# Kernel tuning notes

Measured on AMD Instinct MI355X. Metric: run time of the kernel, lower is better.

The kernel has to match this reference:

```python
import jax, jax.numpy as jnp
import numpy as np

B, S, D, H = 4, 2048, 1024, 16
HD = D // H


def sinusoidal_pe(max_len, d_model):
    pos = np.arange(max_len)[:, None].astype(np.float32)
    div = np.exp(np.arange(0, d_model, 2).astype(np.float32) * (-np.log(10000.0) / d_model))
    pe = np.zeros((max_len, d_model), dtype=np.float32)
    pe[:, 0::2] = np.sin(pos * div)
    pe[:, 1::2] = np.cos(pos * div)
    return jnp.asarray(pe)


def setup_inputs() -> dict:
    key = jax.random.key(0)
    ks = jax.random.split(key, 9)
    s = 1.0 / np.sqrt(D)
    inp = {
        "x": jax.random.normal(ks[0], (B, S, D), dtype=jnp.float32),
        "Wq": jax.random.normal(ks[1], (D, D), dtype=jnp.float32) * s,
        "bq": jnp.zeros((D,), dtype=jnp.float32),
        "Wk": jax.random.normal(ks[2], (D, D), dtype=jnp.float32) * s,
        "bk": jnp.zeros((D,), dtype=jnp.float32),
        "Wv": jax.random.normal(ks[3], (D, D), dtype=jnp.float32) * s,
        "bv": jnp.zeros((D,), dtype=jnp.float32),
        "Wp": jax.random.normal(ks[4], (D, D), dtype=jnp.float32) * s,
        "bp": jnp.zeros((D,), dtype=jnp.float32),
        "pe": sinusoidal_pe(S, D),
    }
    return inp


def reference(x, Wq, bq, Wk, bk, Wv, bv, Wp, bp, pe):
    # positional encoding (eval mode: dropout is identity)
    xp = x + pe[None, :, :]  # [B,S,D]
    split = lambda t: t.reshape(B, S, H, HD).transpose(0, 2, 1, 3)  # [B,H,S,HD]
    q = split(xp @ Wq.T + bq)
    k = split(xp @ Wk.T + bk)
    v = split(xp @ Wv.T + bv)
    scores = jnp.einsum("bhqd,bhkd->bhqk", q, k) / jnp.sqrt(jnp.float32(HD))
    attn = jax.nn.softmax(scores, axis=-1)
    ctx = jnp.einsum("bhqk,bhkd->bhqd", attn, v)
    ctx = ctx.transpose(0, 2, 1, 3).reshape(B, S, D)
    return ctx @ Wp.T + bp
```

## Files before the change

kernel.cpp:

```cpp
#include <hip/hip_runtime.h>
#include <hip/hip_bf16.h>
#include <stdint.h>

#define B_  4
#define S_  2048
#define D_  1024
#define H_  16
#define HD_ 64

typedef __bf16 bfx8   __attribute__((ext_vector_type(8)));
typedef float  f32x4  __attribute__((ext_vector_type(4)));
typedef float  f32x16 __attribute__((ext_vector_type(16)));
typedef short  s16x4  __attribute__((ext_vector_type(4)));
typedef float  fl4    __attribute__((ext_vector_type(4)));
typedef unsigned int u32x2 __attribute__((ext_vector_type(2)));
typedef unsigned int u32x4 __attribute__((ext_vector_type(4)));

#define EXP2(x) __builtin_amdgcn_exp2f(x)

static __device__ __forceinline__ unsigned short f2bf(float f) {
    union { float f; unsigned int u; } v; v.f = f;
    unsigned int r = v.u + 0x7fffu + ((v.u >> 16) & 1u);
    return (unsigned short)(r >> 16);
}
static __device__ __forceinline__ unsigned int fbits(float f) {
    union { float f; unsigned int u; } v; v.f = f; return v.u;
}

#define GLD_LDS16(gp, lp) __builtin_amdgcn_global_load_lds( \
    (const __attribute__((address_space(1))) unsigned int*)(gp), \
    (__attribute__((address_space(3))) unsigned int*)(lp), 16, 0, 0)

__global__ __launch_bounds__(256) void prep_kernel(
    const float* __restrict__ x, const float* __restrict__ pe,
    const float* __restrict__ w0, const float* __restrict__ w1,
    const float* __restrict__ w2, const float* __restrict__ w3,
    unsigned short* __restrict__ xpb, unsigned short* __restrict__ wcat)
{
    const int blk = blockIdx.x;
    if (blk < 8192) {
        int i = (blk * 256 + threadIdx.x) * 4;
        fl4 xv = *(const fl4*)(x + i);
        fl4 pv = *(const fl4*)(pe + (i & (S_ * D_ - 1)));
        s16x4 r;
#pragma unroll
        for (int j = 0; j < 4; j++) r[j] = (short)f2bf(xv[j] + pv[j]);
        *(s16x4*)(xpb + i) = r;
    } else {
        const int bb = blk - 8192;
        const int wsel = bb >> 10;
        const float* src = wsel == 0 ? w0 : wsel == 1 ? w1 : wsel == 2 ? w2 : w3;
        int i = (((bb & 1023) * 256) + threadIdx.x) * 4;
        fl4 v = *(const fl4*)(src + i);
        s16x4 r;
#pragma unroll
        for (int j = 0; j < 4; j++) r[j] = (short)f2bf(v[j]);
        *(s16x4*)(wcat + (size_t)wsel * D_ * D_ + i) = r;
    }
}

__global__ __launch_bounds__(256, 2) void gemm_qkv(
    const unsigned short* __restrict__ A,
    const unsigned short* __restrict__ Bw,
    const float* __restrict__ bq, const float* __restrict__ bk,
    const float* __restrict__ bv,
    unsigned short* __restrict__ Qo, unsigned short* __restrict__ Ko,
    unsigned short* __restrict__ Vo, float qscale)
{
    constexpr int K = D_;
    __shared__ unsigned short As[128 * 32];
    __shared__ unsigned short Bs[128 * 32];
    const int hw  = blockIdx.x;
    const int xcd = hw & 7;
    const int i_  = hw >> 3;
    const int m0  = (i_ / 3) * 128;
    const int n0  = (xcd * 3 + i_ % 3) * 128;

    const int t  = threadIdx.x;
    const int l  = t & 63;
    const int w  = t >> 6;
    const int wr = (w >> 1) * 64;
    const int wc = (w & 1) * 64;
    const int lr = l & 15;
    const int lg = l >> 4;
    const int lk = lg * 8;

    const int e0 = t * 8;
    const int sr = e0 >> 5;
    const int sc = e0 & 31;
    const unsigned short* pA = A  + (size_t)(m0 + sr) * K + sc;
    const unsigned short* pB = Bw + (size_t)(n0 + sr) * K + sc;

    f32x4 acc[4][4] = {};

    for (int k0 = 0; k0 < K; k0 += 32) {
        __syncthreads();
        GLD_LDS16(pA + k0,                    As + e0);
        GLD_LDS16(pA + k0 + (size_t)64 * K,   As + 2048 + e0);
        GLD_LDS16(pB + k0,                    Bs + e0);
        GLD_LDS16(pB + k0 + (size_t)64 * K,   Bs + 2048 + e0);
        __syncthreads();
        bfx8 af[4], bf[4];
#pragma unroll
        for (int i = 0; i < 4; i++)
            af[i] = *(const bfx8*)(As + (wr + i * 16 + lr) * 32 + lk);
#pragma unroll
        for (int i = 0; i < 4; i++)
            bf[i] = *(const bfx8*)(Bs + (wc + i * 16 + lr) * 32 + lk);
#pragma unroll
        for (int i = 0; i < 4; i++)
#pragma unroll
            for (int j = 0; j < 4; j++)
                acc[i][j] = __builtin_amdgcn_mfma_f32_16x16x32_bf16(
                    af[i], bf[j], acc[i][j], 0, 0, 0);
    }

    const int sel = n0 >> 10;
    const float* bias = sel == 0 ? bq : sel == 1 ? bk : bv;
    const float osc = sel == 0 ? qscale : 1.0f;

#pragma unroll
    for (int i = 0; i < 4; i++) {
        const int row0 = m0 + wr + i * 16 + lg * 4;
#pragma unroll
        for (int j = 0; j < 4; j++) {
            const int colf = n0 + wc + j * 16 + lr;
            const int ocol = colf & 1023;
            const float bvv = bias[ocol];
            if (sel < 2) {
                unsigned short* C = sel == 0 ? Qo : Ko;
#pragma unroll
                for (int v = 0; v < 4; v++)
                    C[(size_t)(row0 + v) * D_ + ocol] = f2bf((acc[i][j][v] + bvv) * osc);
            } else {
                const int bidx = row0 >> 11;
                const int s0   = row0 & (S_ - 1);
                s16x4 r;
#pragma unroll
                for (int v = 0; v < 4; v++) r[v] = (short)f2bf(acc[i][j][v] + bvv);
                *(s16x4*)(Vo + (size_t)(bidx * D_ + ocol) * S_ + s0) = r;
            }
        }
    }
}

__global__ __launch_bounds__(256, 2) void gemm_out(
    const unsigned short* __restrict__ A,
    const unsigned short* __restrict__ Bw,
    const float* __restrict__ bias,
    float* __restrict__ Cout)
{
    constexpr int K = D_;
    constexpr int N = D_;
    __shared__ unsigned short As[128 * 32];
    __shared__ unsigned short Bs[128 * 32];
    const int hw = blockIdx.x;
    const int logical = (hw & 7) * 64 + (hw >> 3);
    const int m0 = (logical >> 3) * 128;
    const int n0 = (logical & 7) * 128;

    const int t  = threadIdx.x;
    const int l  = t & 63;
    const int w  = t >> 6;
    const int wr = (w >> 1) * 64;
    const int wc = (w & 1) * 64;
    const int lr = l & 15;
    const int lg = l >> 4;
    const int lk = lg * 8;

    const int e0 = t * 8;
    const int sr = e0 >> 5;
    const int sc = e0 & 31;
    const unsigned short* pA = A  + (size_t)(m0 + sr) * K + sc;
    const unsigned short* pB = Bw + (size_t)(n0 + sr) * K + sc;

    f32x4 acc[4][4] = {};

    for (int k0 = 0; k0 < K; k0 += 32) {
        __syncthreads();
        GLD_LDS16(pA + k0,                    As + e0);
        GLD_LDS16(pA + k0 + (size_t)64 * K,   As + 2048 + e0);
        GLD_LDS16(pB + k0,                    Bs + e0);
        GLD_LDS16(pB + k0 + (size_t)64 * K,   Bs + 2048 + e0);
        __syncthreads();
        bfx8 af[4], bf[4];
#pragma unroll
        for (int i = 0; i < 4; i++)
            af[i] = *(const bfx8*)(As + (wr + i * 16 + lr) * 32 + lk);
#pragma unroll
        for (int i = 0; i < 4; i++)
            bf[i] = *(const bfx8*)(Bs + (wc + i * 16 + lr) * 32 + lk);
#pragma unroll
        for (int i = 0; i < 4; i++)
#pragma unroll
            for (int j = 0; j < 4; j++)
                acc[i][j] = __builtin_amdgcn_mfma_f32_16x16x32_bf16(
                    af[i], bf[j], acc[i][j], 0, 0, 0);
    }

#pragma unroll
    for (int i = 0; i < 4; i++) {
        const int row0 = m0 + wr + i * 16 + lg * 4;
#pragma unroll
        for (int j = 0; j < 4; j++) {
            const int col = n0 + wc + j * 16 + lr;
            const float bv = bias[col];
#pragma unroll
            for (int v = 0; v < 4; v++)
                Cout[(size_t)(row0 + v) * N + col] = acc[i][j][v] + bv;
        }
    }
}

__global__ __launch_bounds__(256, 4) void attn_kernel(
    const unsigned short* __restrict__ Qb,
    const unsigned short* __restrict__ Kb,
    const unsigned short* __restrict__ Vt,
    unsigned short* __restrict__ Ctx)
{
    __shared__ __align__(16) unsigned short Ks[2][64 * 64];
    __shared__ __align__(16) unsigned short Vs[2][64 * 64];

    const int hw = blockIdx.x;
    const int logical = (hw & 7) * 128 + (hw >> 3);
    const int bh = logical >> 4;
    const int t  = threadIdx.x;
    const int l  = t & 63;
    const int w  = t >> 6;
    const int b  = bh >> 4;
    const int h  = bh & 15;
    const int lr = l & 31;
    const int hi = l >> 5;
    const int q0 = (logical & 15) * 128 + w * 32;

    const unsigned short* Qbase = Qb + (size_t)b * S_ * D_ + h * HD_;
    const unsigned short* Kbase = Kb + (size_t)b * S_ * D_ + h * HD_;
    const unsigned short* Vbase = Vt + (size_t)bh * HD_ * S_;

    const int r0  = t >> 3;
    const int cgs = (t & 7) ^ (r0 & 7);
    const unsigned short* Ksrc0 = Kbase + (size_t)r0 * D_ + cgs * 8;
    const unsigned short* Ksrc1 = Kbase + (size_t)(r0 + 32) * D_ + cgs * 8;
    const unsigned short* Vsrc0 = Vbase + (size_t)r0 * S_ + cgs * 8;
    const unsigned short* Vsrc1 = Vbase + (size_t)(r0 + 32) * S_ + cgs * 8;
    const int ld0 = t * 8, ld1 = t * 8 + 2048;

    GLD_LDS16(Ksrc0, &Ks[0][ld0]);
    GLD_LDS16(Ksrc1, &Ks[0][ld1]);
    GLD_LDS16(Vsrc0, &Vs[0][ld0]);
    GLD_LDS16(Vsrc1, &Vs[0][ld1]);

    bfx8 qf[4];
#pragma unroll
    for (int t4 = 0; t4 < 4; t4++)
        qf[t4] = *(const bfx8*)(Qbase + (size_t)(q0 + lr) * D_ + t4 * 16 + hi * 8);

    f32x16 acc0 = {}, acc1 = {};
    float l_r = 0.f;
    const int sw = lr & 7;

    int cur = 0;
    for (int ki = 0; ki < S_ / 64; ki++) {
        __syncthreads();
        if (ki + 1 < S_ / 64) {
            GLD_LDS16(Ksrc0 + (size_t)(ki + 1) * 64 * D_, &Ks[cur ^ 1][ld0]);
            GLD_LDS16(Ksrc1 + (size_t)(ki + 1) * 64 * D_, &Ks[cur ^ 1][ld1]);
            GLD_LDS16(Vsrc0 + (ki + 1) * 64,              &Vs[cur ^ 1][ld0]);
            GLD_LDS16(Vsrc1 + (ki + 1) * 64,              &Vs[cur ^ 1][ld1]);
        }
        const unsigned short* Kc = Ks[cur];
        const unsigned short* Vc = Vs[cur];

        f32x16 s0 = {}, s1 = {};
        __builtin_amdgcn_s_setprio(1);
#pragma unroll
        for (int t4 = 0; t4 < 4; t4++) {
            const int ch = ((t4 * 2 + hi) ^ sw) * 8;
            bfx8 a0 = *(const bfx8*)(Kc + lr * 64 + ch);
            bfx8 a1 = *(const bfx8*)(Kc + (32 + lr) * 64 + ch);
            s0 = __builtin_amdgcn_mfma_f32_32x32x16_bf16(a0, qf[t4], s0, 0, 0, 0);
            s1 = __builtin_amdgcn_mfma_f32_32x32x16_bf16(a1, qf[t4], s1, 0, 0, 0);
        }
        __builtin_amdgcn_s_setprio(0);

        float c0 = 0.f, c1 = 0.f, c2 = 0.f, c3 = 0.f;
#pragma unroll
        for (int r = 0; r < 16; r += 4) {
            float p0 = EXP2(s0[r]);     s0[r] = p0;     c0 += p0;
            float p1 = EXP2(s0[r + 1]); s0[r + 1] = p1; c1 += p1;
            float p2 = EXP2(s0[r + 2]); s0[r + 2] = p2; c2 += p2;
            float p3 = EXP2(s0[r + 3]); s0[r + 3] = p3; c3 += p3;
        }
#pragma unroll
        for (int r = 0; r < 16; r += 4) {
            float p0 = EXP2(s1[r]);     s1[r] = p0;     c0 += p0;
            float p1 = EXP2(s1[r + 1]); s1[r + 1] = p1; c1 += p1;
            float p2 = EXP2(s1[r + 2]); s1[r + 2] = p2; c2 += p2;
            float p3 = EXP2(s1[r + 3]); s1[r + 3] = p3; c3 += p3;
        }
        l_r += (c0 + c1) + (c2 + c3);

        unsigned pk0[8], pk1[8];
#pragma unroll
        for (int i = 0; i < 8; i++) {
            pk0[i] = __builtin_amdgcn_perm(fbits(s0[2 * i + 1]), fbits(s0[2 * i]), 0x07060302u);
            pk1[i] = __builtin_amdgcn_perm(fbits(s1[2 * i + 1]), fbits(s1[2 * i]), 0x07060302u);
        }

#pragma unroll
        for (int ks = 0; ks < 4; ks++) {
            const int c = (ks & 1) * 4;
            const unsigned pa0 = (ks >> 1) ? pk1[c]     : pk0[c];
            const unsigned pa1 = (ks >> 1) ? pk1[c + 1] : pk0[c + 1];
            const unsigned pa2 = (ks >> 1) ? pk1[c + 2] : pk0[c + 2];
            const unsigned pa3 = (ks >> 1) ? pk1[c + 3] : pk0[c + 3];
            u32x2 r02 = __builtin_amdgcn_permlane32_swap(pa0, pa2, false, false);
            u32x2 r13 = __builtin_amdgcn_permlane32_swap(pa1, pa3, false, false);
            u32x4 bfr;
            bfr[0] = r02[0];
            bfr[1] = r13[0];
            bfr[2] = r02[1];
            bfr[3] = r13[1];
            union { u32x4 u; bfx8 b; } cvt; cvt.u = bfr;

            const int ch = ((ks * 2 + hi) ^ sw) * 8;
            bfx8 v0 = *(const bfx8*)(Vc + lr * 64 + ch);
            bfx8 v1 = *(const bfx8*)(Vc + (32 + lr) * 64 + ch);
            __builtin_amdgcn_s_setprio(1);
            acc0 = __builtin_amdgcn_mfma_f32_32x32x16_bf16(v0, cvt.b, acc0, 0, 0, 0);
            acc1 = __builtin_amdgcn_mfma_f32_32x32x16_bf16(v1, cvt.b, acc1, 0, 0, 0);
            __builtin_amdgcn_s_setprio(0);
        }
        cur ^= 1;
    }

    const float l_tot = l_r + __shfl_xor(l_r, 32);
    const float rinv = 1.0f / l_tot;
    unsigned short* Cb = Ctx + (size_t)b * S_ * D_ + (size_t)(q0 + lr) * D_ + h * HD_;
#pragma unroll
    for (int dt = 0; dt < 2; dt++)
#pragma unroll
        for (int a = 0; a < 4; a++) {
            s16x4 rv;
#pragma unroll
            for (int v = 0; v < 4; v++)
                rv[v] = (short)f2bf((dt ? acc1[4 * a + v] : acc0[4 * a + v]) * rinv);
            *(s16x4*)(Cb + dt * 32 + 8 * a + 4 * hi) = rv;
        }
}

extern "C" void kernel_launch(void* const* d_in, const int* in_sizes, int n_in,
                              void* d_out, int out_size, void* d_ws, size_t ws_size,
                              hipStream_t stream)
{
    const float* x  = (const float*)d_in[0];
    const float* Wq = (const float*)d_in[1];
    const float* bq = (const float*)d_in[2];
    const float* Wk = (const float*)d_in[3];
    const float* bk = (const float*)d_in[4];
    const float* Wv = (const float*)d_in[5];
    const float* bv = (const float*)d_in[6];
    const float* Wp = (const float*)d_in[7];
    const float* bp = (const float*)d_in[8];
    const float* pe = (const float*)d_in[9];

    char* ws = (char*)d_ws;
    const size_t MD = (size_t)B_ * S_ * D_;
    unsigned short* xpb = (unsigned short*)ws; ws += MD * 2;
    unsigned short* wqb = (unsigned short*)ws; ws += (size_t)D_ * D_ * 2;
    unsigned short* wkb = (unsigned short*)ws; ws += (size_t)D_ * D_ * 2;
    unsigned short* wvb = (unsigned short*)ws; ws += (size_t)D_ * D_ * 2;
    unsigned short* wpb = (unsigned short*)ws; ws += (size_t)D_ * D_ * 2;
    unsigned short* qb  = (unsigned short*)ws; ws += MD * 2;
    unsigned short* kb  = (unsigned short*)ws; ws += MD * 2;
    unsigned short* vtb = (unsigned short*)ws; ws += MD * 2;
    unsigned short* ctb = (unsigned short*)ws; ws += MD * 2;

    prep_kernel<<<12288, 256, 0, stream>>>(x, pe, Wq, Wk, Wv, Wp, xpb, wqb);

    const float qscale = 0.125f * 1.44269504088896340736f;

    gemm_qkv<<<1536, 256, 0, stream>>>(xpb, wqb, bq, bk, bv, qb, kb, vtb, qscale);

    attn_kernel<<<1024, 256, 0, stream>>>(qb, kb, vtb, ctb);

    gemm_out<<<512, 256, 0, stream>>>(ctb, wpb, bp, (float*)d_out);
}
```

Before: 201.8 us.

## Replace both GEMMs with 256x256 double-buffered, swizzled, phased MFMA kernel

Replaces the 128x128 single-buffered QKV and output GEMMs with one templated kernel. It uses 256x256 tiles, 512 threads and a K step of 64. The LDS buffers are double-buffered with an XOR swizzle. Each k-step is split into four phases that interleave async global-to-LDS loads with MFMA bursts, using explicit barriers and s_setprio. The aim is more data reuse per LDS byte, fewer barriers and better overlap of loads with compute. The cost is fewer blocks: 128 for the output GEMM on a 256-CU part, and about 1.5 waves for QKV. The 128 KB of LDS also limits each CU to one block.

Measured after the change: 210.0 us. 4.1% more time.

```diff
diff --git a/kernel.cpp b/kernel.cpp
--- a/kernel.cpp
+++ b/kernel.cpp
@@ -30,6 +30,10 @@
 #define GLD_LDS16(gp, lp) __builtin_amdgcn_global_load_lds( \
     (const __attribute__((address_space(1))) unsigned int*)(gp), \
     (__attribute__((address_space(3))) unsigned int*)(lp), 16, 0, 0)
+
+#define MFMA16(a, b, c) __builtin_amdgcn_mfma_f32_16x16x32_bf16((a), (b), (c), 0, 0, 0)
+#define SBAR()  do { __builtin_amdgcn_sched_barrier(0); __builtin_amdgcn_s_barrier(); \
+                     __builtin_amdgcn_sched_barrier(0); } while (0)
 
 __global__ __launch_bounds__(256) void prep_kernel(
     const float* __restrict__ x, const float* __restrict__ pe,
@@ -59,157 +63,184 @@
     }
 }
 
-__global__ __launch_bounds__(256, 2) void gemm_qkv(
+template<int MODE>
+__global__ __launch_bounds__(512, 2) void gemm_8ph(
     const unsigned short* __restrict__ A,
     const unsigned short* __restrict__ Bw,
-    const float* __restrict__ bq, const float* __restrict__ bk,
-    const float* __restrict__ bv,
-    unsigned short* __restrict__ Qo, unsigned short* __restrict__ Ko,
-    unsigned short* __restrict__ Vo, float qscale)
+    const float* __restrict__ b0, const float* __restrict__ b1,
+    const float* __restrict__ b2,
+    unsigned short* __restrict__ O0, unsigned short* __restrict__ O1,
+    unsigned short* __restrict__ O2, float* __restrict__ Fo, float qscale)
 {
-    constexpr int K = D_;
-    __shared__ unsigned short As[128 * 32];
-    __shared__ unsigned short Bs[128 * 32];
+    constexpr int KK  = 1024;
+    constexpr int NKT = 16;
+    __shared__ __align__(16) unsigned short As[2][256 * 64];
+    __shared__ __align__(16) unsigned short Bs[2][256 * 64];
+
     const int hw  = blockIdx.x;
     const int xcd = hw & 7;
     const int i_  = hw >> 3;
-    const int m0  = (i_ / 3) * 128;
-    const int n0  = (xcd * 3 + i_ % 3) * 128;
-
-    const int t  = threadIdx.x;
-    const int l  = t & 63;
-    const int w  = t >> 6;
-    const int wr = (w >> 1) * 64;
-    const int wc = (w & 1) * 64;
-    const int lr = l & 15;
-    const int lg = l >> 4;
-    const int lk = lg * 8;
-
-    const int e0 = t * 8;
-    const int sr = e0 >> 5;
-    const int sc = e0 & 31;
-    const unsigned short* pA = A  + (size_t)(m0 + sr) * K + sc;
-    const unsigned short* pB = Bw + (size_t)(n0 + sr) * K + sc;
-
-    f32x4 acc[4][4] = {};
-
-    for (int k0 = 0; k0 < K; k0 += 32) {
-        __syncthreads();
-        GLD_LDS16(pA + k0,                    As + e0);
-        GLD_LDS16(pA + k0 + (size_t)64 * K,   As + 2048 + e0);
-        GLD_LDS16(pB + k0,                    Bs + e0);
-        GLD_LDS16(pB + k0 + (size_t)64 * K,   Bs + 2048 + e0);
-        __syncthreads();
-        bfx8 af[4], bf[4];
+    const int mt  = xcd * 4 + (i_ & 3);
+    const int nt  = i_ >> 2;
+    const int m0  = mt * 256;
+    const int n0  = nt * 256;
+
+    const int t   = threadIdx.x;
+    const int wid = t >> 6;
+    const int wm  = wid >> 2;
+    const int wn  = wid & 3;
+    const int l   = t & 63;
+    const int lr  = l & 15;
+    const int lg  = l >> 4;
+
+    const int srow  = t >> 3;
+    const int sslot = t & 7;
+
+#define STAGE_HALF(dst, X, R0, kn, half) do {                                   \
+    const int r0_ = (half) * 128 + srow;                                        \
+    const int r1_ = r0_ + 64;                                                   \
+    GLD_LDS16(X + (size_t)((R0) + r0_) * KK + (kn) + ((sslot ^ (r0_ & 7)) * 8), \
+              (dst) + 8 * t + (half) * 8192);                                   \
+    GLD_LDS16(X + (size_t)((R0) + r1_) * KK + (kn) + ((sslot ^ (r1_ & 7)) * 8), \
+              (dst) + 8 * t + (half) * 8192 + 4096);                            \
+} while (0)
+
+#define RD(buf, row, ks) \
+    (*(const bfx8*)((buf) + (row) * 64 + ((((ks) * 4 + lg) ^ ((row) & 7)) * 8)))
+
+    f32x4 acc[8][4] = {};
+    bfx8 af[4][2], bfa[2][2], bfb[2][2];
+
+    STAGE_HALF(As[0], A,  m0, 0, 0);
+    STAGE_HALF(As[0], A,  m0, 0, 1);
+    STAGE_HALF(Bs[0], Bw, n0, 0, 0);
+    STAGE_HALF(Bs[0], Bw, n0, 0, 1);
+
+    for (int kt = 0; kt < NKT; ++kt) {
+        const int c = kt & 1;
+        const unsigned short* Ac = As[c];
+        const unsigned short* Bc = Bs[c];
+        unsigned short* An = As[c ^ 1];
+        unsigned short* Bn = Bs[c ^ 1];
+        const int kn = ((kt + 1) & (NKT - 1)) * 64;
+
+        STAGE_HALF(An, A, m0, kn, 0);
+        asm volatile("s_waitcnt vmcnt(2)" ::: "memory");
+        SBAR();
+#pragma unroll
+        for (int i = 0; i < 4; i++) {
+            af[i][0] = RD(Ac, wm * 128 + i * 16 + lr, 0);
+            af[i][1] = RD(Ac, wm * 128 + i * 16 + lr, 1);
+        }
+#pragma unroll
+        for (int j = 0; j < 2; j++) {
+            bfa[j][0] = RD(Bc, wn * 64 + j * 16 + lr, 0);
+            bfa[j][1] = RD(Bc, wn * 64 + j * 16 + lr, 1);
+        }
+        __builtin_amdgcn_s_setprio(1);
 #pragma unroll
         for (int i = 0; i < 4; i++)
-            af[i] = *(const bfx8*)(As + (wr + i * 16 + lr) * 32 + lk);
+#pragma unroll
+            for (int j = 0; j < 2; j++) {
+                acc[i][j] = MFMA16(af[i][0], bfa[j][0], acc[i][j]);
+                acc[i][j] = MFMA16(af[i][1], bfa[j][1], acc[i][j]);
+            }
+        __builtin_amdgcn_s_setprio(0);
+        SBAR();
+
+#pragma unroll
+        for (int j = 0; j < 2; j++) {
+            bfb[j][0] = RD(Bc, wn * 64 + 32 + j * 16 + lr, 0);
+            bfb[j][1] = RD(Bc, wn * 64 + 32 + j * 16 + lr, 1);
+        }
+        STAGE_HALF(An, A, m0, kn, 1);
+        SBAR();
+        __builtin_amdgcn_s_setprio(1);
 #pragma unroll
         for (int i = 0; i < 4; i++)
-            bf[i] = *(const bfx8*)(Bs + (wc + i * 16 + lr) * 32 + lk);
+#pragma unroll
+            for (int j = 0; j < 2; j++) {
+                acc[i][2 + j] = MFMA16(af[i][0], bfb[j][0], acc[i][2 + j]);
+                acc[i][2 + j] = MFMA16(af[i][1], bfb[j][1], acc[i][2 + j]);
+            }
+        __builtin_amdgcn_s_setprio(0);
+        SBAR();
+
+#pragma unroll
+        for (int i = 0; i < 4; i++) {
+            af[i][0] = RD(Ac, wm * 128 + (4 + i) * 16 + lr, 0);
+            af[i][1] = RD(Ac, wm * 128 + (4 + i) * 16 + lr, 1);
+        }
+        STAGE_HALF(Bn, Bw, n0, kn, 0);
+        SBAR();
+        __builtin_amdgcn_s_setprio(1);
 #pragma unroll
         for (int i = 0; i < 4; i++)
 #pragma unroll
-            for (int j = 0; j < 4; j++)
-                acc[i][j] = __builtin_amdgcn_mfma_f32_16x16x32_bf16(
-                    af[i], bf[j], acc[i][j], 0, 0, 0);
+            for (int j = 0; j < 2; j++) {
+                acc[4 + i][j] = MFMA16(af[i][0], bfa[j][0], acc[4 + i][j]);
+                acc[4 + i][j] = MFMA16(af[i][1], bfa[j][1], acc[4 + i][j]);
+            }
+        __builtin_amdgcn_s_setprio(0);
+        SBAR();
+
+        STAGE_HALF(Bn, Bw, n0, kn, 1);
+        SBAR();
+        __builtin_amdgcn_s_setprio(1);
+#pragma unroll
+        for (int i = 0; i < 4; i++)
+#pragma unroll
+            for (int j = 0; j < 2; j++) {
+                acc[4 + i][2 + j] = MFMA16(af[i][0], bfb[j][0], acc[4 + i][2 + j]);
+                acc[4 + i][2 + j] = MFMA16(af[i][1], bfb[j][1], acc[4 + i][2 + j]);
+            }
+        __builtin_amdgcn_s_setprio(0);
+        SBAR();
     }
 
-    const int sel = n0 >> 10;
-    const float* bias = sel == 0 ? bq : sel == 1 ? bk : bv;
-    const float osc = sel == 0 ? qscale : 1.0f;
-
-#pragma unroll
-    for (int i = 0; i < 4; i++) {
-        const int row0 = m0 + wr + i * 16 + lg * 4;
-#pragma unroll
-        for (int j = 0; j < 4; j++) {
-            const int colf = n0 + wc + j * 16 + lr;
-            const int ocol = colf & 1023;
-            const float bvv = bias[ocol];
-            if (sel < 2) {
-                unsigned short* C = sel == 0 ? Qo : Ko;
+    if (MODE == 0) {
+        const int sel = n0 >> 10;
+        const float* bias = sel == 0 ? b0 : sel == 1 ? b1 : b2;
+        const float osc = sel == 0 ? qscale : 1.0f;
+#pragma unroll
+        for (int mi = 0; mi < 8; mi++) {
+            const int row0 = m0 + wm * 128 + mi * 16 + lg * 4;
+#pragma unroll
+            for (int ni = 0; ni < 4; ni++) {
+                const int colf = n0 + wn * 64 + ni * 16 + lr;
+                const int ocol = colf & 1023;
+                const float bvv = bias[ocol];
+                if (sel < 2) {
+                    unsigned short* C = sel == 0 ? O0 : O1;
+#pragma unroll
+                    for (int v = 0; v < 4; v++)
+                        C[(size_t)(row0 + v) * D_ + ocol] = f2bf((acc[mi][ni][v] + bvv) * osc);
+                } else {
+                    const int bidx = row0 >> 11;
+                    const int s0   = row0 & (S_ - 1);
+                    s16x4 r;
+#pragma unroll
+                    for (int v = 0; v < 4; v++) r[v] = (short)f2bf(acc[mi][ni][v] + bvv);
+                    *(s16x4*)(O2 + (size_t)(bidx * D_ + ocol) * S_ + s0) = r;
+                }
+            }
+        }
+    } else {
+#pragma unroll
+        for (int mi = 0; mi < 8; mi++) {
+            const int row0 = m0 + wm * 128 + mi * 16 + lg * 4;
+#pragma unroll
+            for (int ni = 0; ni < 4; ni++) {
+                const int col = n0 + wn * 64 + ni * 16 + lr;
+                const float bvv = b0[col];
 #pragma unroll
                 for (int v = 0; v < 4; v++)
-                    C[(size_t)(row0 + v) * D_ + ocol] = f2bf((acc[i][j][v] + bvv) * osc);
-            } else {
-                const int bidx = row0 >> 11;
-                const int s0   = row0 & (S_ - 1);
-                s16x4 r;
-#pragma unroll
-                for (int v = 0; v < 4; v++) r[v] = (short)f2bf(acc[i][j][v] + bvv);
-                *(s16x4*)(Vo + (size_t)(bidx * D_ + ocol) * S_ + s0) = r;
+                    Fo[(size_t)(row0 + v) * D_ + col] = acc[mi][ni][v] + bvv;
             }
         }
     }
-}
-
-__global__ __launch_bounds__(256, 2) void gemm_out(
-    const unsigned short* __restrict__ A,
-    const unsigned short* __restrict__ Bw,
-    const float* __restrict__ bias,
-    float* __restrict__ Cout)
-{
-    constexpr int K = D_;
-    constexpr int N = D_;
-    __shared__ unsigned short As[128 * 32];
-    __shared__ unsigned short Bs[128 * 32];
-    const int hw = blockIdx.x;
-    const int logical = (hw & 7) * 64 + (hw >> 3);
-    const int m0 = (logical >> 3) * 128;
-    const int n0 = (logical & 7) * 128;
-
-    const int t  = threadIdx.x;
-    const int l  = t & 63;
-    const int w  = t >> 6;
-    const int wr = (w >> 1) * 64;
-    const int wc = (w & 1) * 64;
-    const int lr = l & 15;
-    const int lg = l >> 4;
-    const int lk = lg * 8;
-
-    const int e0 = t * 8;
-    const int sr = e0 >> 5;
-    const int sc = e0 & 31;
-    const unsigned short* pA = A  + (size_t)(m0 + sr) * K + sc;
-    const unsigned short* pB = Bw + (size_t)(n0 + sr) * K + sc;
-
-    f32x4 acc[4][4] = {};
-
-    for (int k0 = 0; k0 < K; k0 += 32) {
-        __syncthreads();
-        GLD_LDS16(pA + k0,                    As + e0);
-        GLD_LDS16(pA + k0 + (size_t)64 * K,   As + 2048 + e0);
-        GLD_LDS16(pB + k0,                    Bs + e0);
-        GLD_LDS16(pB + k0 + (size_t)64 * K,   Bs + 2048 + e0);
-        __syncthreads();
-        bfx8 af[4], bf[4];
-#pragma unroll
-        for (int i = 0; i < 4; i++)
-            af[i] = *(const bfx8*)(As + (wr + i * 16 + lr) * 32 + lk);
-#pragma unroll
-        for (int i = 0; i < 4; i++)
-            bf[i] = *(const bfx8*)(Bs + (wc + i * 16 + lr) * 32 + lk);
-#pragma unroll
-        for (int i = 0; i < 4; i++)
-#pragma unroll
-            for (int j = 0; j < 4; j++)
-                acc[i][j] = __builtin_amdgcn_mfma_f32_16x16x32_bf16(
-                    af[i], bf[j], acc[i][j], 0, 0, 0);
-    }
-
-#pragma unroll
-    for (int i = 0; i < 4; i++) {
-        const int row0 = m0 + wr + i * 16 + lg * 4;
-#pragma unroll
-        for (int j = 0; j < 4; j++) {
-            const int col = n0 + wc + j * 16 + lr;
-            const float bv = bias[col];
-#pragma unroll
-            for (int v = 0; v < 4; v++)
-                Cout[(size_t)(row0 + v) * N + col] = acc[i][j][v] + bv;
-        }
-    }
+#undef STAGE_HALF
+#undef RD
 }
 
 __global__ __launch_bounds__(256, 4) void attn_kernel(
@@ -380,9 +411,11 @@
 
     const float qscale = 0.125f * 1.44269504088896340736f;
 
-    gemm_qkv<<<1536, 256, 0, stream>>>(xpb, wqb, bq, bk, bv, qb, kb, vtb, qscale);
+    gemm_8ph<0><<<384, 512, 0, stream>>>(xpb, wqb, bq, bk, bv,
+                                         qb, kb, vtb, nullptr, qscale);
 
     attn_kernel<<<1024, 256, 0, stream>>>(qb, kb, vtb, ctb);
 
-    gemm_out<<<512, 256, 0, stream>>>(ctb, wpb, bp, (float*)d_out);
-}
+    gemm_8ph<1><<<128, 512, 0, stream>>>(ctb, wpb, bp, nullptr, nullptr,
+                                         nullptr, nullptr, nullptr, (float*)d_out, 1.0f);
+}
```
